# Performance work log

Hardware: AMD Instinct MI355X
Metric: run time of the kernel (lower is better)

The kernel has to match this reference:

```python
import jax, jax.numpy as jnp
import numpy as np

N_LABELS = 301   # vessel labels 1..301; label 0 is background
N_GROUPS = 7     # stands in for RandInt(1, n_groups=10)() in the original
VOL = (256, 256, 256)


def setup_inputs() -> dict:
    key = jax.random.key(0)
    k1, k2, k3 = jax.random.split(key, 3)
    # integer vessel-ID volume (0 = background)
    vessel_labels = jax.random.randint(k1, VOL, 0, N_LABELS + 1, dtype=jnp.int32)
    # stand-ins for the cornucopia random-field transforms (parenchyma_ outputs)
    parenchyma = jax.random.uniform(k2, VOL, jnp.float32, 0.5, 2.0)
    vessel_texture = jax.random.uniform(k3, VOL, jnp.float32, 0.8, 1.2)
    # label -> intensity LUT replicating the grouped masked_fill loop:
    # sorted labels split into N_GROUPS consecutive chunks, each chunk sharing
    # one Uniform(0.25, 0.75) intensity; background (label 0) stays 0.
    per_group = int(np.ceil(N_LABELS / N_GROUPS))
    group_intensity = np.random.RandomState(0).uniform(0.25, 0.75, N_GROUPS).astype(np.float32)
    lut = np.repeat(group_intensity, per_group)[:N_LABELS]
    intensity_lut = jnp.concatenate([jnp.zeros((1,), jnp.float32), jnp.asarray(lut)])
    return {
        "vessel_labels": vessel_labels,
        "parenchyma": parenchyma,
        "vessel_texture": vessel_texture,
        "intensity_lut": intensity_lut,
    }


def reference(vessel_labels, parenchyma, vessel_texture, intensity_lut):
    # vessels_: the per-label masked_fill_ loop collapses into one gather
    scaling = intensity_lut[vessel_labels]          # [X,Y,Z] float32
    vessels = scaling * vessel_texture              # intensity * texture
    vessels = jnp.where(vessels == 0.0, jnp.float32(1.0), vessels)  # vessels[vessels==0]=1
    final_volume = parenchyma * vessels
    vessel_mask = vessel_labels.astype(bool)
    return final_volume, vessel_mask
```

## Files before the change

kernel.cpp:

```cpp
#include <hip/hip_runtime.h>


#define N_ELEMS (256 * 256 * 256)
#define LUT_SIZE 302
#define BLOCK 256
#define CHUNKS 4

typedef float vfloat4 __attribute__((ext_vector_type(4)));
typedef int   vint4   __attribute__((ext_vector_type(4)));

__global__ __launch_bounds__(BLOCK) void octvolsynth_kernel(
    const int* __restrict__ labels,
    const float* __restrict__ parenchyma,
    const float* __restrict__ texture,
    const float* __restrict__ lut,
    float* __restrict__ out)
{
    __shared__ float s_lut[LUT_SIZE];
    const int t = threadIdx.x;
    for (int i = t; i < LUT_SIZE; i += BLOCK) s_lut[i] = lut[i];
    __syncthreads();

    const int base = blockIdx.x * (BLOCK * CHUNKS) + t;

    const vint4*   l4p = (const vint4*)labels;
    const vfloat4* p4p = (const vfloat4*)parenchyma;
    const vfloat4* x4p = (const vfloat4*)texture;

    vint4 l4[CHUNKS];
#pragma unroll
    for (int c = 0; c < CHUNKS; ++c) l4[c] = l4p[base + c * BLOCK];

    vfloat4 p4[CHUNKS], x4[CHUNKS];
#pragma unroll
    for (int c = 0; c < CHUNKS; ++c) p4[c] = p4p[base + c * BLOCK];
#pragma unroll
    for (int c = 0; c < CHUNKS; ++c) x4[c] = x4p[base + c * BLOCK];

    float s[CHUNKS][4];
#pragma unroll
    for (int c = 0; c < CHUNKS; ++c) {
        s[c][0] = s_lut[l4[c].x];
        s[c][1] = s_lut[l4[c].y];
        s[c][2] = s_lut[l4[c].z];
        s[c][3] = s_lut[l4[c].w];
    }

#pragma unroll
    for (int c = 0; c < CHUNKS; ++c) {
        vfloat4 fv, mv;
        float v0 = s[c][0] * x4[c].x;
        float v1 = s[c][1] * x4[c].y;
        float v2 = s[c][2] * x4[c].z;
        float v3 = s[c][3] * x4[c].w;
        fv.x = p4[c].x * ((v0 == 0.0f) ? 1.0f : v0);
        fv.y = p4[c].y * ((v1 == 0.0f) ? 1.0f : v1);
        fv.z = p4[c].z * ((v2 == 0.0f) ? 1.0f : v2);
        fv.w = p4[c].w * ((v3 == 0.0f) ? 1.0f : v3);
        mv.x = (l4[c].x != 0) ? 1.0f : 0.0f;
        mv.y = (l4[c].y != 0) ? 1.0f : 0.0f;
        mv.z = (l4[c].z != 0) ? 1.0f : 0.0f;
        mv.w = (l4[c].w != 0) ? 1.0f : 0.0f;
        __builtin_nontemporal_store(fv, (vfloat4*)out + (base + c * BLOCK));
        __builtin_nontemporal_store(mv, (vfloat4*)(out + N_ELEMS) + (base + c * BLOCK));
    }
}

extern "C" void kernel_launch(void* const* d_in, const int* in_sizes, int n_in,
                              void* d_out, int out_size, void* d_ws, size_t ws_size,
                              hipStream_t stream) {
    const int*   labels     = (const int*)d_in[0];
    const float* parenchyma = (const float*)d_in[1];
    const float* texture    = (const float*)d_in[2];
    const float* lut        = (const float*)d_in[3];
    float* out = (float*)d_out;

    const int n_vec = N_ELEMS / 4;
    const int grid  = n_vec / (BLOCK * CHUNKS);
    octvolsynth_kernel<<<grid, BLOCK, 0, stream>>>(labels, parenchyma, texture, lut, out);
}
```

Measured before the change: 284.2 us.

## Switch to fixed-grid grid-stride loop with register double-buffered prefetch

Replaces the one-shot kernel, where each block handled four chunks, with a fixed grid of 2048 blocks. Each block runs a grid-stride loop of eight iterations and prefetches the next iteration's labels, parenchyma and texture into registers while computing the current one. This amortizes the per-block shared LUT load and syncthreads over more work and keeps loads in flight. The trade-off is fewer independent loads in flight per thread at any one time than the fully unrolled four-chunk version. It also adds a min-blocks-per-SM launch bound, which may constrain registers.

```diff
diff --git a/kernel.cpp b/kernel.cpp
--- a/kernel.cpp
+++ b/kernel.cpp
@@ -2,14 +2,17 @@
 
 
 #define N_ELEMS (256 * 256 * 256)
+#define N_VEC   (N_ELEMS / 4)
 #define LUT_SIZE 302
 #define BLOCK 256
-#define CHUNKS 4
+#define GRID 2048
+#define STRIDE (BLOCK * GRID)
+#define ITERS (N_VEC / STRIDE)
 
 typedef float vfloat4 __attribute__((ext_vector_type(4)));
 typedef int   vint4   __attribute__((ext_vector_type(4)));
 
-__global__ __launch_bounds__(BLOCK) void octvolsynth_kernel(
+__global__ __launch_bounds__(BLOCK, 8) void octvolsynth_kernel(
     const int* __restrict__ labels,
     const float* __restrict__ parenchyma,
     const float* __restrict__ texture,
@@ -21,48 +24,48 @@
     for (int i = t; i < LUT_SIZE; i += BLOCK) s_lut[i] = lut[i];
     __syncthreads();
 
-    const int base = blockIdx.x * (BLOCK * CHUNKS) + t;
-
     const vint4*   l4p = (const vint4*)labels;
     const vfloat4* p4p = (const vfloat4*)parenchyma;
     const vfloat4* x4p = (const vfloat4*)texture;
+    vfloat4* o0 = (vfloat4*)out;
+    vfloat4* o1 = (vfloat4*)(out + N_ELEMS);
 
-    vint4 l4[CHUNKS];
-#pragma unroll
-    for (int c = 0; c < CHUNKS; ++c) l4[c] = l4p[base + c * BLOCK];
+    int idx = blockIdx.x * BLOCK + t;
 
-    vfloat4 p4[CHUNKS], x4[CHUNKS];
-#pragma unroll
-    for (int c = 0; c < CHUNKS; ++c) p4[c] = p4p[base + c * BLOCK];
-#pragma unroll
-    for (int c = 0; c < CHUNKS; ++c) x4[c] = x4p[base + c * BLOCK];
-
-    float s[CHUNKS][4];
-#pragma unroll
-    for (int c = 0; c < CHUNKS; ++c) {
-        s[c][0] = s_lut[l4[c].x];
-        s[c][1] = s_lut[l4[c].y];
-        s[c][2] = s_lut[l4[c].z];
-        s[c][3] = s_lut[l4[c].w];
-    }
+    vint4   l = l4p[idx];
+    vfloat4 p = p4p[idx];
+    vfloat4 x = x4p[idx];
 
 #pragma unroll
-    for (int c = 0; c < CHUNKS; ++c) {
+    for (int i = 0; i < ITERS; ++i) {
+        const vint4   lc = l;
+        const vfloat4 pc = p;
+        const vfloat4 xc = x;
+        const int cur = idx;
+        idx += STRIDE;
+        if (i + 1 < ITERS) {
+            l = l4p[idx];
+            p = p4p[idx];
+            x = x4p[idx];
+        }
+
+        float v0 = s_lut[lc.x] * xc.x;
+        float v1 = s_lut[lc.y] * xc.y;
+        float v2 = s_lut[lc.z] * xc.z;
+        float v3 = s_lut[lc.w] * xc.w;
+
         vfloat4 fv, mv;
-        float v0 = s[c][0] * x4[c].x;
-        float v1 = s[c][1] * x4[c].y;
-        float v2 = s[c][2] * x4[c].z;
-        float v3 = s[c][3] * x4[c].w;
-        fv.x = p4[c].x * ((v0 == 0.0f) ? 1.0f : v0);
-        fv.y = p4[c].y * ((v1 == 0.0f) ? 1.0f : v1);
-        fv.z = p4[c].z * ((v2 == 0.0f) ? 1.0f : v2);
-        fv.w = p4[c].w * ((v3 == 0.0f) ? 1.0f : v3);
-        mv.x = (l4[c].x != 0) ? 1.0f : 0.0f;
-        mv.y = (l4[c].y != 0) ? 1.0f : 0.0f;
-        mv.z = (l4[c].z != 0) ? 1.0f : 0.0f;
-        mv.w = (l4[c].w != 0) ? 1.0f : 0.0f;
-        __builtin_nontemporal_store(fv, (vfloat4*)out + (base + c * BLOCK));
-        __builtin_nontemporal_store(mv, (vfloat4*)(out + N_ELEMS) + (base + c * BLOCK));
+        fv.x = pc.x * ((v0 == 0.0f) ? 1.0f : v0);
+        fv.y = pc.y * ((v1 == 0.0f) ? 1.0f : v1);
+        fv.z = pc.z * ((v2 == 0.0f) ? 1.0f : v2);
+        fv.w = pc.w * ((v3 == 0.0f) ? 1.0f : v3);
+        mv.x = (lc.x != 0) ? 1.0f : 0.0f;
+        mv.y = (lc.y != 0) ? 1.0f : 0.0f;
+        mv.z = (lc.z != 0) ? 1.0f : 0.0f;
+        mv.w = (lc.w != 0) ? 1.0f : 0.0f;
+
+        __builtin_nontemporal_store(fv, o0 + cur);
+        __builtin_nontemporal_store(mv, o1 + cur);
     }
 }
 
@@ -75,7 +78,5 @@
     const float* lut        = (const float*)d_in[3];
     float* out = (float*)d_out;
 
-    const int n_vec = N_ELEMS / 4;
-    const int grid  = n_vec / (BLOCK * CHUNKS);
-    octvolsynth_kernel<<<grid, BLOCK, 0, stream>>>(labels, parenchyma, texture, lut, out);
+    octvolsynth_kernel<<<GRID, BLOCK, 0, stream>>>(labels, parenchyma, texture, lut, out);
 }
```

After: 283.0 us. No clear change (-0.4%).
